# Performance work log

Hardware: AMD Instinct MI355X
Metric: run time of the kernel (lower is better)

The kernel has to match this reference:

```python
import jax, jax.numpy as jnp
import numpy as np

WS = (5, 5, 5, 5)  # 4D window

def _rel_index(ws):
    # faithful port of WindowAttention.relative_bias_4d
    coords = np.stack(np.meshgrid(*[np.arange(w) for w in ws], indexing='ij'))  # (4, H,W,Hs,Ws)
    flat = coords.reshape(len(ws), -1)                       # (4, N)
    rel = (flat[:, :, None] - flat[:, None, :]).transpose(1, 2, 0).astype(np.int64)  # (N, N, 4)
    rel = rel + np.array([ws[0] - 1, ws[1] - 1, ws[2] - 1, ws[3] - 1])
    rel[..., 0] *= (2 * ws[0] - 1) ** 3
    rel[..., 1] *= (2 * ws[1] - 1) ** 2
    rel[..., 2] *= (2 * ws[2] - 1)
    return rel.sum(-1)  # (N, N), values in [0, (2w-1)^4)


def setup_inputs() -> dict:
    key = jax.random.key(0)
    ks = jax.random.split(key, 7)
    dim, heads = 128, 4
    B_, nW = 64, 32
    N = 5 ** 4  # 625
    tbl = (2 * 5 - 1) ** 4  # 6561
    inp = {
        'x': jax.random.normal(ks[0], (B_, N, dim), jnp.float32),
        'mask': jax.random.normal(ks[1], (nW, N, N), jnp.float32),
        'qkv_w': jax.random.normal(ks[2], (3 * dim, dim), jnp.float32) * 0.02,
        'qkv_b': jax.random.normal(ks[3], (3 * dim,), jnp.float32) * 0.02,
        'proj_w': jax.random.normal(ks[4], (dim, dim), jnp.float32) * 0.02,
        'proj_b': jax.random.normal(ks[5], (dim,), jnp.float32) * 0.02,
        'bias_table': jax.random.normal(ks[6], (tbl, heads), jnp.float32) * 0.02,
        'rel_index': jnp.asarray(_rel_index(WS), jnp.int32),
    }
    return inp


def reference(x, mask, qkv_w, qkv_b, proj_w, proj_b, bias_table, rel_index):
    B_, N, C = x.shape
    H = bias_table.shape[-1]
    D = C // H
    scale = D ** -0.5
    # qkv projection -> (3, B_, H, N, D)
    qkv = (x @ qkv_w.T + qkv_b).reshape(B_, N, 3, H, D).transpose(2, 0, 3, 1, 4)
    q, k, v = qkv[0], qkv[1], qkv[2]
    attn = jnp.einsum('bhnd,bhmd->bhnm', q * scale, k)       # (B_, H, N, N)
    bias = bias_table[rel_index].transpose(2, 0, 1)          # (H, N, N)
    attn = attn + bias[None]
    nW = mask.shape[0]
    attn = attn.reshape(B_ // nW, nW, H, N, N) + mask[None, :, None]
    attn = jax.nn.softmax(attn.reshape(B_, H, N, N), axis=-1)
    out = jnp.einsum('bhnm,bhmd->bhnd', attn, v)             # (B_, H, N, D)
    out = out.transpose(0, 2, 1, 3).reshape(B_, N, C)
    return out @ proj_w.T + proj_b
```

## Files before the change

kernel.cpp:

```cpp
#include <hip/hip_runtime.h>
#include <stdint.h>

typedef __attribute__((ext_vector_type(8))) __bf16 bf16x8;
typedef __attribute__((ext_vector_type(4))) __bf16 bf16x4;
typedef __attribute__((ext_vector_type(4))) float f32x4;

#define DEV __device__ __forceinline__
#define LOG2E 1.4426950408889634f
#define SCALE 0.17677669529663687f

static constexpr size_t OFF_Q     = 0;
static constexpr size_t OFF_K     = 10485760;
static constexpr size_t OFF_VT    = 20971520;
static constexpr size_t OFF_O     = 31457280;
static constexpr size_t OFF_BIASP = 41697280;
static constexpr size_t OFF_WBF   = 44974080;

DEV bf16x8 cvt8(const float* p) {
  f32x4 a = *(const f32x4*)p;
  f32x4 b = *(const f32x4*)(p + 4);
  bf16x8 r;
  r[0]=(__bf16)a[0]; r[1]=(__bf16)a[1]; r[2]=(__bf16)a[2]; r[3]=(__bf16)a[3];
  r[4]=(__bf16)b[0]; r[5]=(__bf16)b[1]; r[6]=(__bf16)b[2]; r[7]=(__bf16)b[3];
  return r;
}

DEV f32x4 mfma16(bf16x8 a, bf16x8 b, f32x4 c) {
  return __builtin_amdgcn_mfma_f32_16x16x32_bf16(a, b, c, 0, 0, 0);
}

DEV uint32_t cvtpk(float lo, float hi) {
  uint32_t d;
  asm("v_cvt_pk_bf16_f32 %0, %1, %2" : "=v"(d) : "v"(lo), "v"(hi));
  return d;
}

union U8 { uint32_t u[4]; bf16x8 v; };
union V8 { bf16x4 h[2]; bf16x8 v; };

__global__ __launch_bounds__(256) void k_prep(const float* __restrict__ table,
                                              const int* __restrict__ rel,
                                              __bf16* __restrict__ bp,
                                              __bf16* __restrict__ qp,
                                              __bf16* __restrict__ kp,
                                              __bf16* __restrict__ vp,
                                              const float* __restrict__ wq,
                                              const float* __restrict__ wp,
                                              __bf16* __restrict__ wbf) {
  int blk = blockIdx.x;
  if (blk < 1600) {
    int t = blk * 256 + threadIdx.x;
    int h = t / 102400, rem = t % 102400;
    int i = rem / 160, q = rem % 160;
    int e0 = q * 4;
    int tile = e0 >> 5;
    int ein = e0 & 31;
    int g = ein >> 3, s0 = ein & 7;
    bf16x4 v;
    #pragma unroll
    for (int s2 = 0; s2 < 4; ++s2) {
      int s = s0 + s2;
      int col = 4 * g + (s < 4 ? s : s + 12);
      int j = tile * 32 + col;
      v[s2] = (i < 625 && j < 625)
                ? (__bf16)(table[(size_t)rel[(size_t)i * 625 + j] * 4 + h] * LOG2E)
                : (__bf16)0.f;
    }
    *(bf16x4*)(bp + ((size_t)h * 640 + i) * 640 + e0) = v;
  } else if (blk < 2560) {
    int t = (blk - 1600) * 256 + threadIdx.x;
    const int PAD1 = 256 * 15 * 32;
    if (t < PAD1) {
      int bh = t / 480, rem = t % 480;
      int row = 625 + rem / 32, d = rem & 31;
      size_t idx = ((size_t)bh * 640 + row) * 32 + d;
      qp[idx] = (__bf16)0.f;
      kp[idx] = (__bf16)0.f;
    } else {
      t -= PAD1;
      if (t < PAD1) {
        int bh = t / 480, rem = t % 480;
        int d = rem / 15, col = 625 + rem % 15;
        vp[((size_t)bh * 32 + d) * 640 + col] = (__bf16)0.f;
      }
    }
  } else {
    int t = (blk - 2560) * 256 + threadIdx.x;
    if (t < 49152) wbf[t] = (__bf16)wq[t];
    else           wbf[t] = (__bf16)wp[t - 49152];
  }
}

__global__ __launch_bounds__(256) void k_qkv(const float* __restrict__ x,
                                             const __bf16* __restrict__ wbf,
                                             const float* __restrict__ bias,
                                             __bf16* __restrict__ qp,
                                             __bf16* __restrict__ kp,
                                             __bf16* __restrict__ vp) {
  int lane = threadIdx.x & 63, wv = threadIdx.x >> 6;
  int g = lane >> 4, l15 = lane & 15;
  int row0 = (blockIdx.x * 4 + wv) * 16;

  bf16x8 a[4];
  #pragma unroll
  for (int ks = 0; ks < 4; ++ks)
    a[ks] = cvt8(x + (size_t)(row0 + l15) * 128 + ks * 32 + g * 8);

  #pragma unroll 1
  for (int nf = 0; nf < 24; ++nf) {
    f32x4 acc = {0.f, 0.f, 0.f, 0.f};
    int col = nf * 16 + l15;
    #pragma unroll
    for (int ks = 0; ks < 4; ++ks) {
      bf16x8 bfr = *(const bf16x8*)(wbf + (size_t)col * 128 + ks * 32 + g * 8);
      acc = mfma16(a[ks], bfr, acc);
    }
    float bv = bias[col];
    int which = nf >> 3;
    int h = (col >> 5) & 3, d = col & 31;
    #pragma unroll
    for (int r = 0; r < 4; ++r) {
      int row = row0 + 4 * g + r;
      int b_ = row / 625;
      int n = row - b_ * 625;
      float v = acc[r] + bv;
      size_t bh = (size_t)b_ * 4 + h;
      if (which == 0)       qp[(bh * 640 + n) * 32 + d] = (__bf16)(v * (SCALE * LOG2E));
      else if (which == 1)  kp[(bh * 640 + n) * 32 + d] = (__bf16)v;
      else                  vp[(bh * 32 + d) * 640 + n] = (__bf16)v;
    }
  }
}

__global__ __launch_bounds__(256, 4) void k_attn9(const __bf16* __restrict__ qball,
                                                  const __bf16* __restrict__ kball,
                                                  const __bf16* __restrict__ vball,
                                                  __bf16* __restrict__ oball,
                                                  const __bf16* __restrict__ biasp,
                                                  const float* __restrict__ maskraw) {
  const int tid = threadIdx.x;
  const int lane = tid & 63, wv = tid >> 6;
  const int g = lane >> 4, l15 = lane & 15;
  const bool lowg = (g < 2);

  const int bid = blockIdx.x;
  const int xcd = bid & 7, s = bid >> 3;
  const int w = xcd + 8 * (s & 3);
  const int r_ = s >> 2;
  const int o = r_ & 1, chunk = r_ >> 1;
  const int b = o * 32 + w;
  const int h = wv;
  const size_t bh = (size_t)b * 4 + h;
  const int i0 = chunk * 32;

  const __bf16* qp = qball + bh * (640 * 32);
  const __bf16* kp = kball + bh * (640 * 32);
  const __bf16* vp = vball + bh * (32 * 640);
  const float* maskw = maskraw + (size_t)w * 390625;

  const __bf16* kbase  = kp + (size_t)l15 * 32 + g * 8;
  const int vjoff = 16 * (g >> 1) + 4 * (g & 1);
  const __bf16* vbase0 = vp + (size_t)l15 * 640 + vjoff;
  const __bf16* vbase1 = vp + (size_t)(16 + l15) * 640 + vjoff;
  const __bf16* brow0  = biasp + (size_t)h * 409600 + (size_t)(i0 + l15) * 640 + g * 8;
  const __bf16* brow1  = brow0 + 16 * 640;

  int ia = i0 + l15;       const int ir0 = ia < 625 ? ia : 624;
  int ib_ = i0 + 16 + l15; const int ir1 = ib_ < 625 ? ib_ : 624;
  const float* mrow0 = maskw + (size_t)ir0 * 625 + 4 * g;
  const float* mrow1 = maskw + (size_t)ir1 * 625 + 4 * g;

  bf16x8 aq0 = *(const bf16x8*)(qp + (size_t)(i0 + l15) * 32 + g * 8);
  bf16x8 aq1 = *(const bf16x8*)(qp + (size_t)(i0 + 16 + l15) * 32 + g * 8);

  f32x4 O00 = {0,0,0,0}, O01 = {0,0,0,0}, O10 = {0,0,0,0}, O11 = {0,0,0,0};
  float L0 = 0.f, L1 = 0.f;

  bf16x8 K0, K1;
  bf16x8 B0, B1;
  f32x4 C00, C01, C10, C11;

  C00 = *(const f32x4*)(mrow0);
  C01 = *(const f32x4*)(mrow0 + 16);
  C10 = *(const f32x4*)(mrow1);
  C11 = *(const f32x4*)(mrow1 + 16);
  K0  = *(const bf16x8*)(kbase);
  K1  = *(const bf16x8*)(kbase + 512);
  B0  = *(const bf16x8*)(brow0);
  B1  = *(const bf16x8*)(brow1);

#define SOFTPV(T)                                                              \
  {                                                                            \
    V8 va, vb;                                                                 \
    va.h[0] = *(const bf16x4*)(vbase0 + (T) * 32);                             \
    va.h[1] = *(const bf16x4*)(vbase0 + (T) * 32 + 8);                         \
    vb.h[0] = *(const bf16x4*)(vbase1 + (T) * 32);                             \
    vb.h[1] = *(const bf16x4*)(vbase1 + (T) * 32 + 8);                         \
    float ps0 = 0.f, ps1 = 0.f;                                                \
    f32x4 P00, P01, P10, P11;                                                  \
    _Pragma("unroll")                                                          \
    for (int r = 0; r < 4; ++r) {                                              \
      P00[r] = exp2f(S00[r]);                                                  \
      P01[r] = exp2f(S01[r]);                                                  \
      P10[r] = exp2f(S10[r]);                                                  \
      P11[r] = exp2f(S11[r]);                                                  \
      ps0 += P00[r] + P01[r];                                                  \
      ps1 += P10[r] + P11[r];                                                  \
    }                                                                          \
    L0 += ps0; L1 += ps1;                                                      \
    uint32_t d0 = cvtpk(P00[0], P00[1]);                                       \
    uint32_t d1 = cvtpk(P00[2], P00[3]);                                       \
    uint32_t d2 = cvtpk(P01[0], P01[1]);                                       \
    uint32_t d3 = cvtpk(P01[2], P01[3]);                                       \
    uint32_t e0 = cvtpk(P10[0], P10[1]);                                       \
    uint32_t e1 = cvtpk(P10[2], P10[3]);                                       \
    uint32_t e2 = cvtpk(P11[0], P11[1]);                                       \
    uint32_t e3 = cvtpk(P11[2], P11[3]);                                       \
    uint32_t z0 = lowg ? d2 : d0;                                              \
    uint32_t z1 = lowg ? d3 : d1;                                              \
    uint32_t z2 = lowg ? e2 : e0;                                              \
    uint32_t z3 = lowg ? e3 : e1;                                              \
    uint32_t x0 = __shfl_xor(z0, 32);                                          \
    uint32_t x1 = __shfl_xor(z1, 32);                                          \
    uint32_t x2 = __shfl_xor(z2, 32);                                          \
    uint32_t x3 = __shfl_xor(z3, 32);                                          \
    U8 pa0, pa1;                                                               \
    pa0.u[0] = lowg ? d0 : x0;                                                 \
    pa0.u[1] = lowg ? d1 : x1;                                                 \
    pa0.u[2] = lowg ? x0 : d2;                                                 \
    pa0.u[3] = lowg ? x1 : d3;                                                 \
    pa1.u[0] = lowg ? e0 : x2;                                                 \
    pa1.u[1] = lowg ? e1 : x3;                                                 \
    pa1.u[2] = lowg ? x2 : e2;                                                 \
    pa1.u[3] = lowg ? x3 : e3;                                                 \
    O00 = mfma16(pa0.v, va.v, O00);                                            \
    O01 = mfma16(pa0.v, vb.v, O01);                                            \
    O10 = mfma16(pa1.v, va.v, O10);                                            \
    O11 = mfma16(pa1.v, vb.v, O11);                                            \
  }

  #pragma unroll 1
  for (int t = 0; t < 19; ++t) {
    f32x4 c00, c01, c10, c11;
    #pragma unroll
    for (int r = 0; r < 4; ++r) {
      c00[r] = fmaf(C00[r], LOG2E, (float)B0[r]);
      c01[r] = fmaf(C01[r], LOG2E, (float)B0[4 + r]);
      c10[r] = fmaf(C10[r], LOG2E, (float)B1[r]);
      c11[r] = fmaf(C11[r], LOG2E, (float)B1[4 + r]);
    }
    f32x4 S00 = mfma16(K0, aq0, c00);
    f32x4 S01 = mfma16(K1, aq0, c01);
    f32x4 S10 = mfma16(K0, aq1, c10);
    f32x4 S11 = mfma16(K1, aq1, c11);
    if (t < 18) {
      C00 = *(const f32x4*)(mrow0 + (t + 1) * 32);
      C01 = *(const f32x4*)(mrow0 + (t + 1) * 32 + 16);
      C10 = *(const f32x4*)(mrow1 + (t + 1) * 32);
      C11 = *(const f32x4*)(mrow1 + (t + 1) * 32 + 16);
    }
    K0 = *(const bf16x8*)(kbase + (size_t)(t + 1) * 1024);
    K1 = *(const bf16x8*)(kbase + (size_t)(t + 1) * 1024 + 512);
    B0 = *(const bf16x8*)(brow0 + (t + 1) * 32);
    B1 = *(const bf16x8*)(brow1 + (t + 1) * 32);

    SOFTPV(t)
  }

  {
    const float* mr0 = maskw + (size_t)ir0 * 625;
    const float* mr1 = maskw + (size_t)ir1 * 625;
    f32x4 c, S00, S01, S10, S11;
    #pragma unroll
    for (int r = 0; r < 4; ++r)
      c[r] = fmaf(mr0[608 + 4 * g + r], LOG2E, (float)B0[r]);
    S00 = mfma16(K0, aq0, c);
    #pragma unroll
    for (int r = 0; r < 4; ++r) {
      int j = 624 + 4 * g + r;
      c[r] = (j < 625) ? fmaf(mr0[j], LOG2E, (float)B0[4 + r]) : -1.0e30f;
    }
    S01 = mfma16(K1, aq0, c);
    #pragma unroll
    for (int r = 0; r < 4; ++r)
      c[r] = fmaf(mr1[608 + 4 * g + r], LOG2E, (float)B1[r]);
    S10 = mfma16(K0, aq1, c);
    #pragma unroll
    for (int r = 0; r < 4; ++r) {
      int j = 624 + 4 * g + r;
      c[r] = (j < 625) ? fmaf(mr1[j], LOG2E, (float)B1[4 + r]) : -1.0e30f;
    }
    S11 = mfma16(K1, aq1, c);

    SOFTPV(19)
  }
#undef SOFTPV

  L0 += __shfl_xor(L0, 16); L0 += __shfl_xor(L0, 32);
  L1 += __shfl_xor(L1, 16); L1 += __shfl_xor(L1, 32);
  float inv0 = 1.0f / L0, inv1 = 1.0f / L1;
  f32x4 iv0, iv1;
  #pragma unroll
  for (int r = 0; r < 4; ++r) {
    iv0[r] = __shfl(inv0, 4 * g + r);
    iv1[r] = __shfl(inv1, 4 * g + r);
  }
  #pragma unroll
  for (int r = 0; r < 4; ++r) {
    int ia2 = i0 + 4 * g + r;
    if (ia2 < 625) {
      size_t base = ((size_t)b * 625 + ia2) * 128 + h * 32;
      oball[base + l15]      = (__bf16)(O00[r] * iv0[r]);
      oball[base + 16 + l15] = (__bf16)(O01[r] * iv0[r]);
    }
    int ib2 = i0 + 16 + 4 * g + r;
    if (ib2 < 625) {
      size_t base = ((size_t)b * 625 + ib2) * 128 + h * 32;
      oball[base + l15]      = (__bf16)(O10[r] * iv1[r]);
      oball[base + 16 + l15] = (__bf16)(O11[r] * iv1[r]);
    }
  }
}

__global__ __launch_bounds__(256) void k_proj(const __bf16* __restrict__ obf,
                                              const __bf16* __restrict__ wbf,
                                              const float* __restrict__ bias,
                                              float* __restrict__ out) {
  int lane = threadIdx.x & 63, wv = threadIdx.x >> 6;
  int g = lane >> 4, l15 = lane & 15;
  int row0 = (blockIdx.x * 4 + wv) * 16;

  bf16x8 a[4];
  #pragma unroll
  for (int ks = 0; ks < 4; ++ks)
    a[ks] = *(const bf16x8*)(obf + (size_t)(row0 + l15) * 128 + ks * 32 + g * 8);

  #pragma unroll 1
  for (int nf = 0; nf < 8; ++nf) {
    f32x4 acc = {0.f, 0.f, 0.f, 0.f};
    int col = nf * 16 + l15;
    #pragma unroll
    for (int ks = 0; ks < 4; ++ks) {
      bf16x8 bfr = *(const bf16x8*)(wbf + (size_t)col * 128 + ks * 32 + g * 8);
      acc = mfma16(a[ks], bfr, acc);
    }
    float bv = bias[col];
    #pragma unroll
    for (int r = 0; r < 4; ++r)
      out[(size_t)(row0 + 4 * g + r) * 128 + col] = acc[r] + bv;
  }
}

extern "C" void kernel_launch(void* const* d_in, const int* in_sizes, int n_in,
                              void* d_out, int out_size, void* d_ws, size_t ws_size,
                              hipStream_t stream) {
  (void)in_sizes; (void)n_in; (void)out_size; (void)ws_size;
  const float* x      = (const float*)d_in[0];
  const float* mask   = (const float*)d_in[1];
  const float* qkv_w  = (const float*)d_in[2];
  const float* qkv_b  = (const float*)d_in[3];
  const float* proj_w = (const float*)d_in[4];
  const float* proj_b = (const float*)d_in[5];
  const float* table  = (const float*)d_in[6];
  const int*   rel    = (const int*)d_in[7];
  char* ws = (char*)d_ws;
  float* out = (float*)d_out;

  __bf16* qp    = (__bf16*)(ws + OFF_Q);
  __bf16* kp    = (__bf16*)(ws + OFF_K);
  __bf16* vp    = (__bf16*)(ws + OFF_VT);
  __bf16* obf   = (__bf16*)(ws + OFF_O);
  __bf16* biasp = (__bf16*)(ws + OFF_BIASP);
  __bf16* wbf   = (__bf16*)(ws + OFF_WBF);

  k_prep<<<2816, 256, 0, stream>>>(table, rel, biasp, qp, kp, vp, qkv_w, proj_w, wbf);
  k_qkv<<<625, 256, 0, stream>>>(x, wbf, qkv_b, qp, kp, vp);
  k_attn9<<<1280, 256, 0, stream>>>(qp, kp, vp, obf, biasp, mask);
  k_proj<<<625, 256, 0, stream>>>(obf, wbf + 49152, proj_b, out);
}
```

Measured before the change: 178.0 us.

## Prepack mask into padded tiled layout and use permlane32 swap for P

Adds a prep stage that copies the mask into a padded, tile-major fp32 buffer that is prescaled by log2e and holds -1e30 in the padding. The attention kernel can then run a uniform 20-iteration loop with aligned vector mask loads and no special tail block. The shuffle-and-select used to rearrange the softmax probabilities is replaced by v_permlane32_swap. In exchange, the full 32x625x625 mask is read and rewritten every call, adding roughly 100MB of extra memory traffic in the prep kernel.

```diff
diff --git a/kernel.cpp b/kernel.cpp
--- a/kernel.cpp
+++ b/kernel.cpp
@@ -15,6 +15,7 @@
 static constexpr size_t OFF_O     = 31457280;
 static constexpr size_t OFF_BIASP = 41697280;
 static constexpr size_t OFF_WBF   = 44974080;
+static constexpr size_t OFF_MASKP = 45105152;
 
 DEV bf16x8 cvt8(const float* p) {
   f32x4 a = *(const f32x4*)p;
@@ -46,10 +47,28 @@
                                               __bf16* __restrict__ vp,
                                               const float* __restrict__ wq,
                                               const float* __restrict__ wp,
-                                              __bf16* __restrict__ wbf) {
+                                              __bf16* __restrict__ wbf,
+                                              const float* __restrict__ mask,
+                                              float* __restrict__ mpk) {
   int blk = blockIdx.x;
-  if (blk < 1600) {
-    int t = blk * 256 + threadIdx.x;
+  if (blk < 12800) {
+    int t4 = blk * 256 + threadIdx.x;
+    int jq = (t4 & 7) * 4;
+    int rest = t4 >> 3;
+    int i = rest % 640;
+    int rest2 = rest / 640;
+    int tt = rest2 % 20;
+    int w = rest2 / 20;
+    const float* src = mask + (size_t)w * 390625 + (size_t)i * 625;
+    f32x4 v;
+    #pragma unroll
+    for (int r = 0; r < 4; ++r) {
+      int j = tt * 32 + jq + r;
+      v[r] = (i < 625 && j < 625) ? src[j] * LOG2E : -1.0e30f;
+    }
+    *(f32x4*)(mpk + (((size_t)w * 20 + tt) * 640 + i) * 32 + jq) = v;
+  } else if (blk < 14400) {
+    int t = (blk - 12800) * 256 + threadIdx.x;
     int h = t / 102400, rem = t % 102400;
     int i = rem / 160, q = rem % 160;
     int e0 = q * 4;
@@ -67,8 +86,8 @@
                 : (__bf16)0.f;
     }
     *(bf16x4*)(bp + ((size_t)h * 640 + i) * 640 + e0) = v;
-  } else if (blk < 2560) {
-    int t = (blk - 1600) * 256 + threadIdx.x;
+  } else if (blk < 15360) {
+    int t = (blk - 14400) * 256 + threadIdx.x;
     const int PAD1 = 256 * 15 * 32;
     if (t < PAD1) {
       int bh = t / 480, rem = t % 480;
@@ -85,7 +104,7 @@
       }
     }
   } else {
-    int t = (blk - 2560) * 256 + threadIdx.x;
+    int t = (blk - 15360) * 256 + threadIdx.x;
     if (t < 49152) wbf[t] = (__bf16)wq[t];
     else           wbf[t] = (__bf16)wp[t - 49152];
   }
@@ -132,16 +151,15 @@
   }
 }
 
-__global__ __launch_bounds__(256, 4) void k_attn9(const __bf16* __restrict__ qball,
-                                                  const __bf16* __restrict__ kball,
-                                                  const __bf16* __restrict__ vball,
-                                                  __bf16* __restrict__ oball,
-                                                  const __bf16* __restrict__ biasp,
-                                                  const float* __restrict__ maskraw) {
+__global__ __launch_bounds__(256, 4) void k_attn10(const __bf16* __restrict__ qball,
+                                                   const __bf16* __restrict__ kball,
+                                                   const __bf16* __restrict__ vball,
+                                                   __bf16* __restrict__ oball,
+                                                   const __bf16* __restrict__ biasp,
+                                                   const float* __restrict__ maskp) {
   const int tid = threadIdx.x;
   const int lane = tid & 63, wv = tid >> 6;
   const int g = lane >> 4, l15 = lane & 15;
-  const bool lowg = (g < 2);
 
   const int bid = blockIdx.x;
   const int xcd = bid & 7, s = bid >> 3;
@@ -156,7 +174,6 @@
   const __bf16* qp = qball + bh * (640 * 32);
   const __bf16* kp = kball + bh * (640 * 32);
   const __bf16* vp = vball + bh * (32 * 640);
-  const float* maskw = maskraw + (size_t)w * 390625;
 
   const __bf16* kbase  = kp + (size_t)l15 * 32 + g * 8;
   const int vjoff = 16 * (g >> 1) + 4 * (g & 1);
@@ -164,11 +181,8 @@
   const __bf16* vbase1 = vp + (size_t)(16 + l15) * 640 + vjoff;
   const __bf16* brow0  = biasp + (size_t)h * 409600 + (size_t)(i0 + l15) * 640 + g * 8;
   const __bf16* brow1  = brow0 + 16 * 640;
-
-  int ia = i0 + l15;       const int ir0 = ia < 625 ? ia : 624;
-  int ib_ = i0 + 16 + l15; const int ir1 = ib_ < 625 ? ib_ : 624;
-  const float* mrow0 = maskw + (size_t)ir0 * 625 + 4 * g;
-  const float* mrow1 = maskw + (size_t)ir1 * 625 + 4 * g;
+  const float* mrow0 = maskp + ((size_t)w * 20 * 640 + (size_t)(i0 + l15)) * 32 + 4 * g;
+  const float* mrow1 = mrow0 + 16 * 32;
 
   bf16x8 aq0 = *(const bf16x8*)(qp + (size_t)(i0 + l15) * 32 + g * 8);
   bf16x8 aq1 = *(const bf16x8*)(qp + (size_t)(i0 + 16 + l15) * 32 + g * 8);
@@ -189,112 +203,70 @@
   B0  = *(const bf16x8*)(brow0);
   B1  = *(const bf16x8*)(brow1);
 
-#define SOFTPV(T)                                                              \
-  {                                                                            \
-    V8 va, vb;                                                                 \
-    va.h[0] = *(const bf16x4*)(vbase0 + (T) * 32);                             \
-    va.h[1] = *(const bf16x4*)(vbase0 + (T) * 32 + 8);                         \
-    vb.h[0] = *(const bf16x4*)(vbase1 + (T) * 32);                             \
-    vb.h[1] = *(const bf16x4*)(vbase1 + (T) * 32 + 8);                         \
-    float ps0 = 0.f, ps1 = 0.f;                                                \
-    f32x4 P00, P01, P10, P11;                                                  \
-    _Pragma("unroll")                                                          \
-    for (int r = 0; r < 4; ++r) {                                              \
-      P00[r] = exp2f(S00[r]);                                                  \
-      P01[r] = exp2f(S01[r]);                                                  \
-      P10[r] = exp2f(S10[r]);                                                  \
-      P11[r] = exp2f(S11[r]);                                                  \
-      ps0 += P00[r] + P01[r];                                                  \
-      ps1 += P10[r] + P11[r];                                                  \
-    }                                                                          \
-    L0 += ps0; L1 += ps1;                                                      \
-    uint32_t d0 = cvtpk(P00[0], P00[1]);                                       \
-    uint32_t d1 = cvtpk(P00[2], P00[3]);                                       \
-    uint32_t d2 = cvtpk(P01[0], P01[1]);                                       \
-    uint32_t d3 = cvtpk(P01[2], P01[3]);                                       \
-    uint32_t e0 = cvtpk(P10[0], P10[1]);                                       \
-    uint32_t e1 = cvtpk(P10[2], P10[3]);                                       \
-    uint32_t e2 = cvtpk(P11[0], P11[1]);                                       \
-    uint32_t e3 = cvtpk(P11[2], P11[3]);                                       \
-    uint32_t z0 = lowg ? d2 : d0;                                              \
-    uint32_t z1 = lowg ? d3 : d1;                                              \
-    uint32_t z2 = lowg ? e2 : e0;                                              \
-    uint32_t z3 = lowg ? e3 : e1;                                              \
-    uint32_t x0 = __shfl_xor(z0, 32);                                          \
-    uint32_t x1 = __shfl_xor(z1, 32);                                          \
-    uint32_t x2 = __shfl_xor(z2, 32);                                          \
-    uint32_t x3 = __shfl_xor(z3, 32);                                          \
-    U8 pa0, pa1;                                                               \
-    pa0.u[0] = lowg ? d0 : x0;                                                 \
-    pa0.u[1] = lowg ? d1 : x1;                                                 \
-    pa0.u[2] = lowg ? x0 : d2;                                                 \
-    pa0.u[3] = lowg ? x1 : d3;                                                 \
-    pa1.u[0] = lowg ? e0 : x2;                                                 \
-    pa1.u[1] = lowg ? e1 : x3;                                                 \
-    pa1.u[2] = lowg ? x2 : e2;                                                 \
-    pa1.u[3] = lowg ? x3 : e3;                                                 \
-    O00 = mfma16(pa0.v, va.v, O00);                                            \
-    O01 = mfma16(pa0.v, vb.v, O01);                                            \
-    O10 = mfma16(pa1.v, va.v, O10);                                            \
-    O11 = mfma16(pa1.v, vb.v, O11);                                            \
-  }
-
   #pragma unroll 1
-  for (int t = 0; t < 19; ++t) {
+  for (int t = 0; t < 20; ++t) {
+    V8 va, vb;
+    va.h[0] = *(const bf16x4*)(vbase0 + t * 32);
+    va.h[1] = *(const bf16x4*)(vbase0 + t * 32 + 8);
+    vb.h[0] = *(const bf16x4*)(vbase1 + t * 32);
+    vb.h[1] = *(const bf16x4*)(vbase1 + t * 32 + 8);
+
     f32x4 c00, c01, c10, c11;
     #pragma unroll
     for (int r = 0; r < 4; ++r) {
-      c00[r] = fmaf(C00[r], LOG2E, (float)B0[r]);
-      c01[r] = fmaf(C01[r], LOG2E, (float)B0[4 + r]);
-      c10[r] = fmaf(C10[r], LOG2E, (float)B1[r]);
-      c11[r] = fmaf(C11[r], LOG2E, (float)B1[4 + r]);
+      c00[r] = C00[r] + (float)B0[r];
+      c01[r] = C01[r] + (float)B0[4 + r];
+      c10[r] = C10[r] + (float)B1[r];
+      c11[r] = C11[r] + (float)B1[4 + r];
     }
     f32x4 S00 = mfma16(K0, aq0, c00);
     f32x4 S01 = mfma16(K1, aq0, c01);
     f32x4 S10 = mfma16(K0, aq1, c10);
     f32x4 S11 = mfma16(K1, aq1, c11);
-    if (t < 18) {
-      C00 = *(const f32x4*)(mrow0 + (t + 1) * 32);
-      C01 = *(const f32x4*)(mrow0 + (t + 1) * 32 + 16);
-      C10 = *(const f32x4*)(mrow1 + (t + 1) * 32);
-      C11 = *(const f32x4*)(mrow1 + (t + 1) * 32 + 16);
-    }
-    K0 = *(const bf16x8*)(kbase + (size_t)(t + 1) * 1024);
-    K1 = *(const bf16x8*)(kbase + (size_t)(t + 1) * 1024 + 512);
-    B0 = *(const bf16x8*)(brow0 + (t + 1) * 32);
-    B1 = *(const bf16x8*)(brow1 + (t + 1) * 32);
-
-    SOFTPV(t)
-  }
-
-  {
-    const float* mr0 = maskw + (size_t)ir0 * 625;
-    const float* mr1 = maskw + (size_t)ir1 * 625;
-    f32x4 c, S00, S01, S10, S11;
-    #pragma unroll
-    for (int r = 0; r < 4; ++r)
-      c[r] = fmaf(mr0[608 + 4 * g + r], LOG2E, (float)B0[r]);
-    S00 = mfma16(K0, aq0, c);
+
+    const int tn = (t < 19) ? t + 1 : 19;
+    C00 = *(const f32x4*)(mrow0 + (size_t)tn * 20480);
+    C01 = *(const f32x4*)(mrow0 + (size_t)tn * 20480 + 16);
+    C10 = *(const f32x4*)(mrow1 + (size_t)tn * 20480);
+    C11 = *(const f32x4*)(mrow1 + (size_t)tn * 20480 + 16);
+    K0 = *(const bf16x8*)(kbase + (size_t)tn * 1024);
+    K1 = *(const bf16x8*)(kbase + (size_t)tn * 1024 + 512);
+    B0 = *(const bf16x8*)(brow0 + tn * 32);
+    B1 = *(const bf16x8*)(brow1 + tn * 32);
+
+    float ps0 = 0.f, ps1 = 0.f;
+    f32x4 P00, P01, P10, P11;
     #pragma unroll
     for (int r = 0; r < 4; ++r) {
-      int j = 624 + 4 * g + r;
-      c[r] = (j < 625) ? fmaf(mr0[j], LOG2E, (float)B0[4 + r]) : -1.0e30f;
-    }
-    S01 = mfma16(K1, aq0, c);
-    #pragma unroll
-    for (int r = 0; r < 4; ++r)
-      c[r] = fmaf(mr1[608 + 4 * g + r], LOG2E, (float)B1[r]);
-    S10 = mfma16(K0, aq1, c);
-    #pragma unroll
-    for (int r = 0; r < 4; ++r) {
-      int j = 624 + 4 * g + r;
-      c[r] = (j < 625) ? fmaf(mr1[j], LOG2E, (float)B1[4 + r]) : -1.0e30f;
-    }
-    S11 = mfma16(K1, aq1, c);
-
-    SOFTPV(19)
-  }
-#undef SOFTPV
+      P00[r] = exp2f(S00[r]);
+      P01[r] = exp2f(S01[r]);
+      P10[r] = exp2f(S10[r]);
+      P11[r] = exp2f(S11[r]);
+      ps0 += P00[r] + P01[r];
+      ps1 += P10[r] + P11[r];
+    }
+    L0 += ps0; L1 += ps1;
+    uint32_t d0 = cvtpk(P00[0], P00[1]);
+    uint32_t d1 = cvtpk(P00[2], P00[3]);
+    uint32_t d2 = cvtpk(P01[0], P01[1]);
+    uint32_t d3 = cvtpk(P01[2], P01[3]);
+    uint32_t e0 = cvtpk(P10[0], P10[1]);
+    uint32_t e1 = cvtpk(P10[2], P10[3]);
+    uint32_t e2 = cvtpk(P11[0], P11[1]);
+    uint32_t e3 = cvtpk(P11[2], P11[3]);
+    asm("v_permlane32_swap_b32 %0, %1" : "+v"(d0), "+v"(d2));
+    asm("v_permlane32_swap_b32 %0, %1" : "+v"(d1), "+v"(d3));
+    asm("v_permlane32_swap_b32 %0, %1" : "+v"(e0), "+v"(e2));
+    asm("v_permlane32_swap_b32 %0, %1" : "+v"(e1), "+v"(e3));
+    U8 pa0, pa1;
+    pa0.u[0] = d0; pa0.u[1] = d1; pa0.u[2] = d2; pa0.u[3] = d3;
+    pa1.u[0] = e0; pa1.u[1] = e1; pa1.u[2] = e2; pa1.u[3] = e3;
+
+    O00 = mfma16(pa0.v, va.v, O00);
+    O01 = mfma16(pa0.v, vb.v, O01);
+    O10 = mfma16(pa1.v, va.v, O10);
+    O11 = mfma16(pa1.v, vb.v, O11);
+  }
 
   L0 += __shfl_xor(L0, 16); L0 += __shfl_xor(L0, 32);
   L1 += __shfl_xor(L1, 16); L1 += __shfl_xor(L1, 32);
@@ -372,9 +344,10 @@
   __bf16* obf   = (__bf16*)(ws + OFF_O);
   __bf16* biasp = (__bf16*)(ws + OFF_BIASP);
   __bf16* wbf   = (__bf16*)(ws + OFF_WBF);
-
-  k_prep<<<2816, 256, 0, stream>>>(table, rel, biasp, qp, kp, vp, qkv_w, proj_w, wbf);
+  float*  mpk   = (float*)(ws + OFF_MASKP);
+
+  k_prep<<<15616, 256, 0, stream>>>(table, rel, biasp, qp, kp, vp, qkv_w, proj_w, wbf, mask, mpk);
   k_qkv<<<625, 256, 0, stream>>>(x, wbf, qkv_b, qp, kp, vp);
-  k_attn9<<<1280, 256, 0, stream>>>(qp, kp, vp, obf, biasp, mask);
+  k_attn10<<<1280, 256, 0, stream>>>(qp, kp, vp, obf, biasp, mpk);
   k_proj<<<625, 256, 0, stream>>>(obf, wbf + 49152, proj_b, out);
 }
```

Result: slower. 225.5 us (+26.7%).
